# Optimization experiments

Hardware: AMD Instinct MI355X
Metric: run time of the kernel (lower is better)

Reference implementation:

```python
import jax, jax.numpy as jnp
import numpy as np

EMB = 1024
HEADS = 16
HEAD_DIM = EMB // HEADS  # 64


def setup_inputs() -> dict:
    key = jax.random.key(0)
    ks = jax.random.split(key, 11)
    B, S = 2, 2048
    scale = 1.0 / np.sqrt(EMB)
    inp = {
        "xv": jax.random.normal(ks[0], (B, S, EMB), jnp.float32),
        "xk": jax.random.normal(ks[1], (B, S, EMB), jnp.float32),
        "xq": jax.random.normal(ks[2], (B, S, EMB), jnp.float32),
        "Wq": jax.random.normal(ks[3], (EMB, EMB), jnp.float32) * scale,
        "bq": jax.random.normal(ks[4], (EMB,), jnp.float32) * 0.01,
        "Wk": jax.random.normal(ks[5], (EMB, EMB), jnp.float32) * scale,
        "bk": jax.random.normal(ks[6], (EMB,), jnp.float32) * 0.01,
        "Wv": jax.random.normal(ks[7], (EMB, EMB), jnp.float32) * scale,
        "bv": jax.random.normal(ks[8], (EMB,), jnp.float32) * 0.01,
        "Wo": jax.random.normal(ks[9], (EMB, EMB), jnp.float32) * scale,
        "bo": jax.random.normal(ks[10], (EMB,), jnp.float32) * 0.01,
    }
    return inp


def reference(xv, xk, xq, Wq, bq, Wk, bk, Wv, bv, Wo, bo):
    B, S, E = xq.shape
    H, D = HEADS, HEAD_DIM
    # projections (x @ W + b), split into heads: [B,S,H,D]
    Q = (xq @ Wq + bq).reshape(B, S, H, D)
    K = (xk @ Wk + bk).reshape(B, S, H, D)
    V = (xv @ Wv + bv).reshape(B, S, H, D)
    # scaled dot-product attention per head (vectorized over heads)
    scores = jnp.einsum("bqhd,bkhd->bhqk", Q, K) / jnp.sqrt(jnp.float32(D))
    attn = jax.nn.softmax(scores, axis=-1)
    ctx = jnp.einsum("bhqk,bkhd->bqhd", attn, V).reshape(B, S, E)
    return ctx @ Wo + bo
```

## Files before the change

### kernel.cpp

```cpp
#include <hip/hip_runtime.h>
#include <hip/hip_bf16.h>

typedef __hip_bfloat16 bf16;
typedef __attribute__((ext_vector_type(8))) short short8;
typedef __attribute__((ext_vector_type(4))) short short4v;
typedef __attribute__((ext_vector_type(4))) float floatx4;

#define MFMA16 __builtin_amdgcn_mfma_f32_16x16x32_bf16


__device__ __forceinline__ void gl16(const void* g, void* l) {
    __builtin_amdgcn_global_load_lds(
        (const __attribute__((address_space(1))) void*)g,
        (__attribute__((address_space(3))) void*)l, 16, 0, 0);
}

__global__ __launch_bounds__(256) void wtrans_k(const float* __restrict__ w0,
                                                const float* __restrict__ w1,
                                                const float* __restrict__ w2,
                                                const float* __restrict__ w3,
                                                bf16* __restrict__ dst) {
    const float* srcs[4] = {w0, w1, w2, w3};
    const float* src = srcs[blockIdx.z];
    bf16* d = dst + (size_t)blockIdx.z * 1024 * 1024;
    __shared__ float t[32][33];
    int tx = threadIdx.x, ty = threadIdx.y;
    int x0 = blockIdx.x * 32, y0 = blockIdx.y * 32;
#pragma unroll
    for (int i = 0; i < 4; i++)
        t[ty + i * 8][tx] = src[(size_t)(y0 + ty + i * 8) * 1024 + x0 + tx];
    __syncthreads();
#pragma unroll
    for (int i = 0; i < 4; i++)
        d[(size_t)(x0 + ty + i * 8) * 1024 + y0 + tx] =
            __float2bfloat16(t[tx][ty + i * 8]);
}

__global__ __launch_bounds__(256) void qkv_k(const float* __restrict__ xq,
                                             const float* __restrict__ xk,
                                             const float* __restrict__ xv,
                                             const bf16* __restrict__ wt,
                                             const float* __restrict__ bq,
                                             const float* __restrict__ bk,
                                             const float* __restrict__ bv,
                                             bf16* __restrict__ Qw,
                                             bf16* __restrict__ Kw,
                                             bf16* __restrict__ Vt) {
    __shared__ __align__(16) float lAf[128 * 32];
    __shared__ __align__(16) bf16 lB[128 * 32];
    int z = blockIdx.z;
    const float* A = (z == 0) ? xq : (z == 1) ? xk : xv;
    const bf16* Bt = wt + (size_t)z * (1024 * 1024);
    const float* bias = (z == 0) ? bq : (z == 1) ? bk : bv;
    int m0 = blockIdx.x * 128, n0 = blockIdx.y * 128;
    int tid = threadIdx.x, wave = tid >> 6, lane = tid & 63;
    int lm = lane & 15, quad = lane >> 4;
    int wm = wave >> 1, wn = wave & 1;
    int s7 = lm & 7;
    int swb = quad ^ ((lm >> 1) & 3);

    floatx4 acc[4][4];
#pragma unroll
    for (int i = 0; i < 4; i++)
#pragma unroll
        for (int j = 0; j < 4; j++) acc[i][j] = (floatx4){0.f, 0.f, 0.f, 0.f};

    for (int kt = 0; kt < 32; kt++) {
#pragma unroll
        for (int q2 = 0; q2 < 4; q2++) {
            int slot0 = wave * 256 + q2 * 64;
            int r = (slot0 + lane) >> 3;
            int c = (lane & 7) ^ (r & 7);
            gl16(&A[(size_t)(m0 + r) * 1024 + kt * 32 + c * 4], &lAf[slot0 * 4]);
        }
#pragma unroll
        for (int q2 = 0; q2 < 2; q2++) {
            int slot0 = wave * 128 + q2 * 64;
            int r = (slot0 + lane) >> 2;
            int c = (lane & 3) ^ ((r >> 1) & 3);
            gl16(&Bt[(size_t)(n0 + r) * 1024 + kt * 32 + c * 8], &lB[slot0 * 8]);
        }
        __syncthreads();

        short8 af[4], bfr[4];
#pragma unroll
        for (int ms = 0; ms < 4; ms++) {
            int r = wm * 64 + ms * 16 + lm;
            float4 a0 = *(const float4*)&lAf[(r * 8 + ((2 * quad) ^ s7)) * 4];
            float4 a1 = *(const float4*)&lAf[(r * 8 + ((2 * quad + 1) ^ s7)) * 4];
            union { __hip_bfloat162 h2[4]; short8 s; } pk;
            pk.h2[0] = __float22bfloat162_rn(make_float2(a0.x, a0.y));
            pk.h2[1] = __float22bfloat162_rn(make_float2(a0.z, a0.w));
            pk.h2[2] = __float22bfloat162_rn(make_float2(a1.x, a1.y));
            pk.h2[3] = __float22bfloat162_rn(make_float2(a1.z, a1.w));
            af[ms] = pk.s;
        }
#pragma unroll
        for (int ns = 0; ns < 4; ns++) {
            int r = wn * 64 + ns * 16 + lm;
            bfr[ns] = *(const short8*)&lB[(r * 4 + swb) * 8];
        }
#pragma unroll
        for (int ms = 0; ms < 4; ms++)
#pragma unroll
            for (int ns = 0; ns < 4; ns++)
                acc[ms][ns] = MFMA16(af[ms], bfr[ns], acc[ms][ns], 0, 0, 0);
        __syncthreads();
    }

    bf16* dstQK = (z == 0) ? Qw : Kw;
    float scale = (z == 0) ? 0.125f : 1.0f;
#pragma unroll
    for (int ms = 0; ms < 4; ms++) {
        int rowb = m0 + wm * 64 + ms * 16 + quad * 4;
        int bb = rowb >> 11, s0 = rowb & 2047;
#pragma unroll
        for (int ns = 0; ns < 4; ns++) {
            int col = n0 + wn * 64 + ns * 16 + lm;
            float bvv = bias[col];
            int hh = col >> 6, d = col & 63;
            if (z < 2) {
#pragma unroll
                for (int rr = 0; rr < 4; rr++) {
                    float v = (acc[ms][ns][rr] + bvv) * scale;
                    dstQK[((((size_t)bb * 16 + hh) * 2048 + s0 + rr) << 6) + d] =
                        __float2bfloat16(v);
                }
            } else {
                short4v pk;
#pragma unroll
                for (int rr = 0; rr < 4; rr++) {
                    bf16 h = __float2bfloat16(acc[ms][ns][rr] + bvv);
                    pk[rr] = *(short*)&h;
                }
                *(short4v*)&Vt[((((size_t)bb * 16 + hh) * 64 + d) << 11) + s0] = pk;
            }
        }
    }
}

__global__ __launch_bounds__(256) void outproj_k(const bf16* __restrict__ ctx,
                                                 const bf16* __restrict__ wot,
                                                 const float* __restrict__ bo,
                                                 float* __restrict__ out) {
    __shared__ __align__(16) bf16 lA[128 * 32];
    __shared__ __align__(16) bf16 lB[64 * 32];
    int m0 = blockIdx.x * 128, n0 = blockIdx.y * 64;
    int tid = threadIdx.x, wave = tid >> 6, lane = tid & 63;
    int lm = lane & 15, quad = lane >> 4;
    int wm = wave >> 1, wn = wave & 1;
    int swb = quad ^ ((lm >> 1) & 3);

    floatx4 acc[4][2];
#pragma unroll
    for (int i = 0; i < 4; i++)
#pragma unroll
        for (int j = 0; j < 2; j++) acc[i][j] = (floatx4){0.f, 0.f, 0.f, 0.f};

    for (int kt = 0; kt < 32; kt++) {
#pragma unroll
        for (int q2 = 0; q2 < 2; q2++) {
            int slot0 = wave * 128 + q2 * 64;
            int r = (slot0 + lane) >> 2;
            int c = (lane & 3) ^ ((r >> 1) & 3);
            gl16(&ctx[(size_t)(m0 + r) * 1024 + kt * 32 + c * 8], &lA[slot0 * 8]);
        }
        {
            int slot0 = wave * 64;
            int r = (slot0 + lane) >> 2;
            int c = (lane & 3) ^ ((r >> 1) & 3);
            gl16(&wot[(size_t)(n0 + r) * 1024 + kt * 32 + c * 8], &lB[slot0 * 8]);
        }
        __syncthreads();

        short8 af[4], bfr[2];
#pragma unroll
        for (int ms = 0; ms < 4; ms++) {
            int r = wm * 64 + ms * 16 + lm;
            af[ms] = *(const short8*)&lA[(r * 4 + swb) * 8];
        }
#pragma unroll
        for (int ns = 0; ns < 2; ns++) {
            int r = wn * 32 + ns * 16 + lm;
            bfr[ns] = *(const short8*)&lB[(r * 4 + swb) * 8];
        }
#pragma unroll
        for (int ms = 0; ms < 4; ms++)
#pragma unroll
            for (int ns = 0; ns < 2; ns++)
                acc[ms][ns] = MFMA16(af[ms], bfr[ns], acc[ms][ns], 0, 0, 0);
        __syncthreads();
    }

#pragma unroll
    for (int ms = 0; ms < 4; ms++) {
        int rowb = m0 + wm * 64 + ms * 16 + quad * 4;
#pragma unroll
        for (int ns = 0; ns < 2; ns++) {
            int col = n0 + wn * 32 + ns * 16 + lm;
            float bvv = bo[col];
#pragma unroll
            for (int rr = 0; rr < 4; rr++)
                out[(size_t)(rowb + rr) * 1024 + col] = acc[ms][ns][rr] + bvv;
        }
    }
}

__global__ __launch_bounds__(256) void attn_k(const bf16* __restrict__ Q,
                                              const bf16* __restrict__ K,
                                              const bf16* __restrict__ Vt,
                                              bf16* __restrict__ ctx) {
    __shared__ __align__(16) bf16 lK[64 * 64];
    __shared__ __align__(16) bf16 lV[64 * 64];
    __shared__ __align__(16) bf16 lP[64 * 72];
    int bh = blockIdx.x, qt = blockIdx.y;
    int b = bh >> 4, h = bh & 15;
    const bf16* Qh = Q + (size_t)bh * (2048 * 64);
    const bf16* Kh = K + (size_t)bh * (2048 * 64);
    const bf16* Vh = Vt + (size_t)bh * (64 * 2048);
    int tid = threadIdx.x, wave = tid >> 6, lane = tid & 63;
    int lm = lane & 15, quad = lane >> 4;
    int s7 = lm & 7;

    int qrow = qt * 64 + wave * 16 + lm;
    short8 qf0 = *(const short8*)&Qh[(size_t)qrow * 64 + quad * 8];
    short8 qf1 = *(const short8*)&Qh[(size_t)qrow * 64 + 32 + quad * 8];

    floatx4 o[4];
#pragma unroll
    for (int i = 0; i < 4; i++) o[i] = (floatx4){0.f, 0.f, 0.f, 0.f};
    float lpart[4] = {0.f, 0.f, 0.f, 0.f};

    for (int kt = 0; kt < 32; kt++) {
#pragma unroll
        for (int q2 = 0; q2 < 2; q2++) {
            int slot0 = wave * 128 + q2 * 64;
            int r = (slot0 + lane) >> 3;
            int c = (lane & 7) ^ (r & 7);
            gl16(&Kh[(size_t)(kt * 64 + r) * 64 + c * 8], &lK[slot0 * 8]);
            gl16(&Vh[(size_t)r * 2048 + kt * 64 + c * 8], &lV[slot0 * 8]);
        }
        __syncthreads();

        floatx4 s[4];
#pragma unroll
        for (int i = 0; i < 4; i++) s[i] = (floatx4){0.f, 0.f, 0.f, 0.f};
#pragma unroll
        for (int ns = 0; ns < 4; ns++) {
            int r = ns * 16 + lm;
            short8 kf0 = *(const short8*)&lK[(r * 8 + (quad ^ s7)) * 8];
            short8 kf1 = *(const short8*)&lK[(r * 8 + ((4 + quad) ^ s7)) * 8];
            s[ns] = MFMA16(qf0, kf0, s[ns], 0, 0, 0);
            s[ns] = MFMA16(qf1, kf1, s[ns], 0, 0, 0);
        }

#pragma unroll
        for (int rr = 0; rr < 4; rr++) {
            float p0 = __expf(s[0][rr]);
            float p1 = __expf(s[1][rr]);
            float p2 = __expf(s[2][rr]);
            float p3 = __expf(s[3][rr]);
            lpart[rr] += (p0 + p1) + (p2 + p3);
            int row = (wave * 16 + quad * 4 + rr) * 72;
            lP[row + lm] = __float2bfloat16(p0);
            lP[row + 16 + lm] = __float2bfloat16(p1);
            lP[row + 32 + lm] = __float2bfloat16(p2);
            lP[row + 48 + lm] = __float2bfloat16(p3);
        }

#pragma unroll
        for (int kk = 0; kk < 2; kk++) {
            short8 pf = *(const short8*)&lP[(wave * 16 + lm) * 72 + kk * 32 + quad * 8];
#pragma unroll
            for (int ns = 0; ns < 4; ns++) {
                int r = ns * 16 + lm;
                short8 vf = *(const short8*)&lV[(r * 8 + ((kk * 4 + quad) ^ s7)) * 8];
                o[ns] = MFMA16(pf, vf, o[ns], 0, 0, 0);
            }
        }
        __syncthreads();
    }

    float inv[4];
#pragma unroll
    for (int rr = 0; rr < 4; rr++) {
        float l = lpart[rr];
        l += __shfl_xor(l, 1, 64);
        l += __shfl_xor(l, 2, 64);
        l += __shfl_xor(l, 4, 64);
        l += __shfl_xor(l, 8, 64);
        inv[rr] = 1.f / l;
    }

#pragma unroll
    for (int ns = 0; ns < 4; ns++) {
        int e = h * 64 + ns * 16 + lm;
#pragma unroll
        for (int rr = 0; rr < 4; rr++) {
            int srow = qt * 64 + wave * 16 + quad * 4 + rr;
            ctx[(size_t)(b * 2048 + srow) * 1024 + e] =
                __float2bfloat16(o[ns][rr] * inv[rr]);
        }
    }
}

extern "C" void kernel_launch(void* const* d_in, const int* in_sizes, int n_in,
                              void* d_out, int out_size, void* d_ws, size_t ws_size,
                              hipStream_t stream) {
    const float* xv = (const float*)d_in[0];
    const float* xk = (const float*)d_in[1];
    const float* xq = (const float*)d_in[2];
    const float* Wq = (const float*)d_in[3];
    const float* bq = (const float*)d_in[4];
    const float* Wk = (const float*)d_in[5];
    const float* bk = (const float*)d_in[6];
    const float* Wv = (const float*)d_in[7];
    const float* bv = (const float*)d_in[8];
    const float* Wo = (const float*)d_in[9];
    const float* bo = (const float*)d_in[10];
    float* out = (float*)d_out;
    bf16* ws = (bf16*)d_ws;

    const size_t MB1 = 1024 * 1024;
    bf16* wt  = ws;
    bf16* Qw  = ws + 4 * MB1;
    bf16* Kw  = ws + 8 * MB1;
    bf16* Vt  = ws + 12 * MB1;
    bf16* ctx = ws + 16 * MB1;

    hipLaunchKernelGGL(wtrans_k, dim3(32, 32, 4), dim3(32, 8), 0, stream,
                       Wq, Wk, Wv, Wo, wt);

    hipLaunchKernelGGL(qkv_k, dim3(32, 8, 3), dim3(256), 0, stream,
                       xq, xk, xv, wt, bq, bk, bv, Qw, Kw, Vt);

    hipLaunchKernelGGL(attn_k, dim3(32, 32), dim3(256), 0, stream, Qw, Kw, Vt, ctx);

    hipLaunchKernelGGL(outproj_k, dim3(32, 16), dim3(256), 0, stream,
                       ctx, wt + 3 * MB1, bo, out);
}
```

Measured before the change: 243.2 us.

## Double-buffer LDS in all GEMMs, use exp2 and MFMA row-sum in attention

The QKV, output-projection and attention kernels now double-buffer their LDS tiles, so the global-to-LDS load of the next k-tile is issued before computing on the current one, with one barrier per iteration. In attention, log2(e) is folded into the Q scale so the exponential becomes a native exp2. S is computed transposed (K as the A operand) so P can be written to LDS as packed 4-wide bf16 stores with an XOR swizzle. The softmax denominator is now an MFMA of P against a ones vector, replacing per-lane sums and shuffle reductions. LDS usage doubles, which may lower occupancy, and the row sum now comes from the bf16-rounded P.

```diff
diff --git a/kernel.cpp b/kernel.cpp
--- a/kernel.cpp
+++ b/kernel.cpp
@@ -46,8 +46,8 @@
                                              bf16* __restrict__ Qw,
                                              bf16* __restrict__ Kw,
                                              bf16* __restrict__ Vt) {
-    __shared__ __align__(16) float lAf[128 * 32];
-    __shared__ __align__(16) bf16 lB[128 * 32];
+    __shared__ __align__(16) float lAf[2][128 * 32];
+    __shared__ __align__(16) bf16 lB[2][128 * 32];
     int z = blockIdx.z;
     const float* A = (z == 0) ? xq : (z == 1) ? xk : xv;
     const bf16* Bt = wt + (size_t)z * (1024 * 1024);
@@ -65,29 +65,38 @@
 #pragma unroll
         for (int j = 0; j < 4; j++) acc[i][j] = (floatx4){0.f, 0.f, 0.f, 0.f};
 
-    for (int kt = 0; kt < 32; kt++) {
+    auto stage = [&](int bufi, int kt) {
 #pragma unroll
         for (int q2 = 0; q2 < 4; q2++) {
             int slot0 = wave * 256 + q2 * 64;
             int r = (slot0 + lane) >> 3;
             int c = (lane & 7) ^ (r & 7);
-            gl16(&A[(size_t)(m0 + r) * 1024 + kt * 32 + c * 4], &lAf[slot0 * 4]);
+            gl16(&A[(size_t)(m0 + r) * 1024 + kt * 32 + c * 4],
+                 &lAf[bufi][slot0 * 4]);
         }
 #pragma unroll
         for (int q2 = 0; q2 < 2; q2++) {
             int slot0 = wave * 128 + q2 * 64;
             int r = (slot0 + lane) >> 2;
             int c = (lane & 3) ^ ((r >> 1) & 3);
-            gl16(&Bt[(size_t)(n0 + r) * 1024 + kt * 32 + c * 8], &lB[slot0 * 8]);
-        }
-        __syncthreads();
+            gl16(&Bt[(size_t)(n0 + r) * 1024 + kt * 32 + c * 8],
+                 &lB[bufi][slot0 * 8]);
+        }
+    };
+
+    stage(0, 0);
+    __syncthreads();
+
+    for (int kt = 0; kt < 32; kt++) {
+        int cur = kt & 1;
+        if (kt < 31) stage(cur ^ 1, kt + 1);
 
         short8 af[4], bfr[4];
 #pragma unroll
         for (int ms = 0; ms < 4; ms++) {
             int r = wm * 64 + ms * 16 + lm;
-            float4 a0 = *(const float4*)&lAf[(r * 8 + ((2 * quad) ^ s7)) * 4];
-            float4 a1 = *(const float4*)&lAf[(r * 8 + ((2 * quad + 1) ^ s7)) * 4];
+            float4 a0 = *(const float4*)&lAf[cur][(r * 8 + ((2 * quad) ^ s7)) * 4];
+            float4 a1 = *(const float4*)&lAf[cur][(r * 8 + ((2 * quad + 1) ^ s7)) * 4];
             union { __hip_bfloat162 h2[4]; short8 s; } pk;
             pk.h2[0] = __float22bfloat162_rn(make_float2(a0.x, a0.y));
             pk.h2[1] = __float22bfloat162_rn(make_float2(a0.z, a0.w));
@@ -98,7 +107,7 @@
 #pragma unroll
         for (int ns = 0; ns < 4; ns++) {
             int r = wn * 64 + ns * 16 + lm;
-            bfr[ns] = *(const short8*)&lB[(r * 4 + swb) * 8];
+            bfr[ns] = *(const short8*)&lB[cur][(r * 4 + swb) * 8];
         }
 #pragma unroll
         for (int ms = 0; ms < 4; ms++)
@@ -109,7 +118,7 @@
     }
 
     bf16* dstQK = (z == 0) ? Qw : Kw;
-    float scale = (z == 0) ? 0.125f : 1.0f;
+    float scale = (z == 0) ? 0.125f * 1.44269504f : 1.0f;
 #pragma unroll
     for (int ms = 0; ms < 4; ms++) {
         int rowb = m0 + wm * 64 + ms * 16 + quad * 4;
@@ -143,8 +152,8 @@
                                                  const bf16* __restrict__ wot,
                                                  const float* __restrict__ bo,
                                                  float* __restrict__ out) {
-    __shared__ __align__(16) bf16 lA[128 * 32];
-    __shared__ __align__(16) bf16 lB[64 * 32];
+    __shared__ __align__(16) bf16 lA[2][128 * 32];
+    __shared__ __align__(16) bf16 lB[2][64 * 32];
     int m0 = blockIdx.x * 128, n0 = blockIdx.y * 64;
     int tid = threadIdx.x, wave = tid >> 6, lane = tid & 63;
     int lm = lane & 15, quad = lane >> 4;
@@ -157,32 +166,41 @@
 #pragma unroll
         for (int j = 0; j < 2; j++) acc[i][j] = (floatx4){0.f, 0.f, 0.f, 0.f};
 
-    for (int kt = 0; kt < 32; kt++) {
+    auto stage = [&](int bufi, int kt) {
 #pragma unroll
         for (int q2 = 0; q2 < 2; q2++) {
             int slot0 = wave * 128 + q2 * 64;
             int r = (slot0 + lane) >> 2;
             int c = (lane & 3) ^ ((r >> 1) & 3);
-            gl16(&ctx[(size_t)(m0 + r) * 1024 + kt * 32 + c * 8], &lA[slot0 * 8]);
+            gl16(&ctx[(size_t)(m0 + r) * 1024 + kt * 32 + c * 8],
+                 &lA[bufi][slot0 * 8]);
         }
         {
             int slot0 = wave * 64;
             int r = (slot0 + lane) >> 2;
             int c = (lane & 3) ^ ((r >> 1) & 3);
-            gl16(&wot[(size_t)(n0 + r) * 1024 + kt * 32 + c * 8], &lB[slot0 * 8]);
-        }
-        __syncthreads();
+            gl16(&wot[(size_t)(n0 + r) * 1024 + kt * 32 + c * 8],
+                 &lB[bufi][slot0 * 8]);
+        }
+    };
+
+    stage(0, 0);
+    __syncthreads();
+
+    for (int kt = 0; kt < 32; kt++) {
+        int cur = kt & 1;
+        if (kt < 31) stage(cur ^ 1, kt + 1);
 
         short8 af[4], bfr[2];
 #pragma unroll
         for (int ms = 0; ms < 4; ms++) {
             int r = wm * 64 + ms * 16 + lm;
-            af[ms] = *(const short8*)&lA[(r * 4 + swb) * 8];
+            af[ms] = *(const short8*)&lA[cur][(r * 4 + swb) * 8];
         }
 #pragma unroll
         for (int ns = 0; ns < 2; ns++) {
             int r = wn * 32 + ns * 16 + lm;
-            bfr[ns] = *(const short8*)&lB[(r * 4 + swb) * 8];
+            bfr[ns] = *(const short8*)&lB[cur][(r * 4 + swb) * 8];
         }
 #pragma unroll
         for (int ms = 0; ms < 4; ms++)
@@ -210,9 +228,9 @@
                                               const bf16* __restrict__ K,
                                               const bf16* __restrict__ Vt,
                                               bf16* __restrict__ ctx) {
-    __shared__ __align__(16) bf16 lK[64 * 64];
-    __shared__ __align__(16) bf16 lV[64 * 64];
-    __shared__ __align__(16) bf16 lP[64 * 72];
+    __shared__ __align__(16) bf16 lK[2][64 * 64];
+    __shared__ __align__(16) bf16 lV[2][64 * 64];
+    __shared__ __align__(16) bf16 lP[64 * 64];
     int bh = blockIdx.x, qt = blockIdx.y;
     int b = bh >> 4, h = bh & 15;
     const bf16* Qh = Q + (size_t)bh * (2048 * 64);
@@ -226,21 +244,34 @@
     short8 qf0 = *(const short8*)&Qh[(size_t)qrow * 64 + quad * 8];
     short8 qf1 = *(const short8*)&Qh[(size_t)qrow * 64 + 32 + quad * 8];
 
+    short8 onesf;
+#pragma unroll
+    for (int i = 0; i < 8; i++) onesf[i] = (short)0x3F80;
+
     floatx4 o[4];
 #pragma unroll
     for (int i = 0; i < 4; i++) o[i] = (floatx4){0.f, 0.f, 0.f, 0.f};
-    float lpart[4] = {0.f, 0.f, 0.f, 0.f};
-
-    for (int kt = 0; kt < 32; kt++) {
+    floatx4 accL = (floatx4){0.f, 0.f, 0.f, 0.f};
+
+    auto stage = [&](int bufi, int kt) {
 #pragma unroll
         for (int q2 = 0; q2 < 2; q2++) {
             int slot0 = wave * 128 + q2 * 64;
             int r = (slot0 + lane) >> 3;
             int c = (lane & 7) ^ (r & 7);
-            gl16(&Kh[(size_t)(kt * 64 + r) * 64 + c * 8], &lK[slot0 * 8]);
-            gl16(&Vh[(size_t)r * 2048 + kt * 64 + c * 8], &lV[slot0 * 8]);
-        }
-        __syncthreads();
+            gl16(&Kh[(size_t)(kt * 64 + r) * 64 + c * 8], &lK[bufi][slot0 * 8]);
+            gl16(&Vh[(size_t)r * 2048 + kt * 64 + c * 8], &lV[bufi][slot0 * 8]);
+        }
+    };
+
+    stage(0, 0);
+    __syncthreads();
+
+    char* lProw = (char*)lP + (wave * 16 + lm) * 128;
+
+    for (int kt = 0; kt < 32; kt++) {
+        int cur = kt & 1;
+        if (kt < 31) stage(cur ^ 1, kt + 1);
 
         floatx4 s[4];
 #pragma unroll
@@ -248,33 +279,34 @@
 #pragma unroll
         for (int ns = 0; ns < 4; ns++) {
             int r = ns * 16 + lm;
-            short8 kf0 = *(const short8*)&lK[(r * 8 + (quad ^ s7)) * 8];
-            short8 kf1 = *(const short8*)&lK[(r * 8 + ((4 + quad) ^ s7)) * 8];
-            s[ns] = MFMA16(qf0, kf0, s[ns], 0, 0, 0);
-            s[ns] = MFMA16(qf1, kf1, s[ns], 0, 0, 0);
-        }
-
-#pragma unroll
-        for (int rr = 0; rr < 4; rr++) {
-            float p0 = __expf(s[0][rr]);
-            float p1 = __expf(s[1][rr]);
-            float p2 = __expf(s[2][rr]);
-            float p3 = __expf(s[3][rr]);
-            lpart[rr] += (p0 + p1) + (p2 + p3);
-            int row = (wave * 16 + quad * 4 + rr) * 72;
-            lP[row + lm] = __float2bfloat16(p0);
-            lP[row + 16 + lm] = __float2bfloat16(p1);
-            lP[row + 32 + lm] = __float2bfloat16(p2);
-            lP[row + 48 + lm] = __float2bfloat16(p3);
+            short8 kf0 = *(const short8*)&lK[cur][(r * 8 + (quad ^ s7)) * 8];
+            short8 kf1 = *(const short8*)&lK[cur][(r * 8 + ((4 + quad) ^ s7)) * 8];
+            s[ns] = MFMA16(kf0, qf0, s[ns], 0, 0, 0);
+            s[ns] = MFMA16(kf1, qf1, s[ns], 0, 0, 0);
+        }
+
+#pragma unroll
+        for (int ns = 0; ns < 4; ns++) {
+            float p0 = __builtin_amdgcn_exp2f(s[ns][0]);
+            float p1 = __builtin_amdgcn_exp2f(s[ns][1]);
+            float p2 = __builtin_amdgcn_exp2f(s[ns][2]);
+            float p3 = __builtin_amdgcn_exp2f(s[ns][3]);
+            union { __hip_bfloat162 h2[2]; short4v s4; } pk;
+            pk.h2[0] = __float22bfloat162_rn(make_float2(p0, p1));
+            pk.h2[1] = __float22bfloat162_rn(make_float2(p2, p3));
+            int sw = (2 * ns + (quad >> 1)) ^ s7;
+            *(short4v*)(lProw + sw * 16 + (quad & 1) * 8) = pk.s4;
         }
 
 #pragma unroll
         for (int kk = 0; kk < 2; kk++) {
-            short8 pf = *(const short8*)&lP[(wave * 16 + lm) * 72 + kk * 32 + quad * 8];
+            int c2 = (kk * 4 + quad) ^ s7;
+            short8 pf = *(const short8*)(lProw + c2 * 16);
+            accL = MFMA16(pf, onesf, accL, 0, 0, 0);
 #pragma unroll
             for (int ns = 0; ns < 4; ns++) {
                 int r = ns * 16 + lm;
-                short8 vf = *(const short8*)&lV[(r * 8 + ((kk * 4 + quad) ^ s7)) * 8];
+                short8 vf = *(const short8*)&lV[cur][(r * 8 + ((kk * 4 + quad) ^ s7)) * 8];
                 o[ns] = MFMA16(pf, vf, o[ns], 0, 0, 0);
             }
         }
@@ -283,14 +315,7 @@
 
     float inv[4];
 #pragma unroll
-    for (int rr = 0; rr < 4; rr++) {
-        float l = lpart[rr];
-        l += __shfl_xor(l, 1, 64);
-        l += __shfl_xor(l, 2, 64);
-        l += __shfl_xor(l, 4, 64);
-        l += __shfl_xor(l, 8, 64);
-        inv[rr] = 1.f / l;
-    }
+    for (int rr = 0; rr < 4; rr++) inv[rr] = 1.f / accL[rr];
 
 #pragma unroll
     for (int ns = 0; ns < 4; ns++) {
```

Result: slower. 255.5 us (+5.0%).
